# Kernel optimization log

Measured on AMD Instinct MI355X. Metric: run time of the kernel, lower is better.

## Reference

```python
import math
import jax, jax.numpy as jnp
import numpy as np

L_LAYERS, H, D, DV, DM, LMAX, V = 4, 16, 1024, 64, 4096, 1024, 32000


def setup_inputs() -> dict:
    key = jax.random.key(0)
    ks = iter(jax.random.split(key, 40))
    def rn(shape, s=0.02):
        return jax.random.normal(next(ks), shape, jnp.float32) * s
    x_ids = jax.random.randint(next(ks), (LMAX,), 0, V)
    return dict(
        x_ids=x_ids,
        word_emb=rn((V, D)), pos_emb=rn((LMAX, D)),
        Wq=rn((L_LAYERS, H, D, D)), bq=jnp.zeros((L_LAYERS, H, D), jnp.float32),
        Wk=rn((L_LAYERS, H, D, D)), bk=jnp.zeros((L_LAYERS, H, D), jnp.float32),
        Wv=rn((L_LAYERS, H, D, DV)), bv=jnp.zeros((L_LAYERS, H, DV), jnp.float32),
        Wo=rn((L_LAYERS, H * DV, D)), bo=jnp.zeros((L_LAYERS, D), jnp.float32),
        g1=rn((L_LAYERS, D), 0.01), b1=rn((L_LAYERS, D), 0.01),
        g2=rn((L_LAYERS, D), 0.01), b2=rn((L_LAYERS, D), 0.01),
        W1=rn((L_LAYERS, D, DM)), bm1=jnp.zeros((L_LAYERS, DM), jnp.float32),
        W2=rn((L_LAYERS, DM, D)), bm2=jnp.zeros((L_LAYERS, D), jnp.float32),
        gf=rn((D,), 0.01), bf=rn((D,), 0.01),
        Wu=rn((D, V)), bu=jnp.zeros((V,), jnp.float32),
    )


def _ln(x, g, b):
    # original normalizes each row over the full embedding vector (biased std)
    mu = jnp.mean(x, axis=-1, keepdims=True)
    sd = jnp.sqrt(jnp.mean((x - mu) ** 2, axis=-1, keepdims=True))
    return g * (x - mu) / sd + b


def reference(x_ids, word_emb, pos_emb, Wq, bq, Wk, bk, Wv, bv, Wo, bo,
              g1, b1, g2, b2, W1, bm1, W2, bm2, gf, bf, Wu, bu):
    x = word_emb[x_ids] + pos_emb[jnp.arange(LMAX)]          # (LMAX, D)
    mask = jnp.tril(jnp.ones((LMAX, LMAX), bool))
    scale = 1.0 / math.sqrt(D)                               # d_attn = d_e
    for l in range(L_LAYERS):
        xn = _ln(x, g1[l], b1[l])
        q = jnp.einsum('ld,hde->hle', xn, Wq[l]) + bq[l][:, None, :]
        k = jnp.einsum('ld,hde->hle', xn, Wk[l]) + bk[l][:, None, :]
        v = jnp.einsum('ld,hdv->hlv', xn, Wv[l]) + bv[l][:, None, :]
        s = jnp.einsum('hqe,hke->hqk', q, k)                 # (H, LMAX, LMAX)
        s = jnp.where(mask, s, -jnp.inf)
        a = jax.nn.softmax(s * scale, axis=-1)
        o = jnp.einsum('hqk,hkv->hqv', a, v)                 # (H, LMAX, DV)
        # faithful reproduction of MHAttention's OVERLAPPING slice writes:
        # head h writes columns [h, h+DV), later heads overwrite earlier ones
        y = jnp.zeros((LMAX, H * DV), x.dtype)
        for h in range(H):
            y = y.at[:, h:h + DV].set(o[h])
        x = x + y @ Wo[l] + bo[l]
        xn2 = _ln(x, g2[l], b2[l])
        # x + act_layer(xn2) where act_layer(z) = z + mlp2(gelu(mlp1(z)))
        x = x + xn2 + jax.nn.gelu(xn2 @ W1[l] + bm1[l]) @ W2[l] + bm2[l]
    x = _ln(x, gf, bf)
    return jax.nn.softmax(x @ Wu + bu, axis=-1)              # (LMAX, V)
```

## Files before the change

### kernel.cpp

```cpp
#include <hip/hip_runtime.h>

typedef __bf16 bf16_t;
typedef __bf16 bf16x8 __attribute__((ext_vector_type(8)));
typedef float f32x4 __attribute__((ext_vector_type(4)));
typedef unsigned int u32;

#define SEQ    1024
#define DEMB   1024
#define NHEAD  16
#define DVDIM  64
#define DMLP   4096
#define NVOCAB 32000
#define NLAYER 4

typedef const __attribute__((address_space(1))) void gas_t;
typedef __attribute__((address_space(3))) void las_t;

__device__ __forceinline__ void gload_lds16(const void* g, void* l) {
  __builtin_amdgcn_global_load_lds((gas_t*)g, (las_t*)l, 16, 0, 0);
}

union PackU { bf16_t h[2]; u32 u; };
union B4U  { uint2 u; bf16_t h[4]; };

__device__ __forceinline__ float blockSum(float v, float* red) {
  #pragma unroll
  for (int o = 32; o > 0; o >>= 1) v += __shfl_down(v, o, 64);
  __syncthreads();
  if ((threadIdx.x & 63) == 0) red[threadIdx.x >> 6] = v;
  __syncthreads();
  return (red[0] + red[1]) + (red[2] + red[3]);
}
__device__ __forceinline__ float blockMax(float v, float* red) {
  #pragma unroll
  for (int o = 32; o > 0; o >>= 1) v = fmaxf(v, __shfl_down(v, o, 64));
  __syncthreads();
  if ((threadIdx.x & 63) == 0) red[threadIdx.x >> 6] = v;
  __syncthreads();
  return fmaxf(fmaxf(red[0], red[1]), fmaxf(red[2], red[3]));
}

__global__ void embed_k(const int* __restrict__ ids, const float* __restrict__ we,
                        const float* __restrict__ pe, float* __restrict__ x) {
  const int row = blockIdx.x, t = threadIdx.x;
  const long id = ids[row];
  float4 a = *(const float4*)(we + id * (long)DEMB + t * 4);
  float4 b = *(const float4*)(pe + (long)row * DEMB + t * 4);
  float4 o; o.x = a.x + b.x; o.y = a.y + b.y; o.z = a.z + b.z; o.w = a.w + b.w;
  *(float4*)(x + (long)row * DEMB + t * 4) = o;
}

__global__ void __launch_bounds__(256)
ln_k(const float* __restrict__ x, const float* __restrict__ g,
     const float* __restrict__ b, bf16_t* __restrict__ xn,
     float* __restrict__ xupd) {
  __shared__ float red[4];
  const int row = blockIdx.x, t = threadIdx.x;
  const float* xr = x + (long)row * DEMB;
  float4 v = *(const float4*)(xr + t * 4);
  float mu = blockSum(v.x + v.y + v.z + v.w, red) * (1.0f / DEMB);
  float dx = v.x - mu, dy = v.y - mu, dz = v.z - mu, dw = v.w - mu;
  float var = blockSum(dx * dx + dy * dy + dz * dz + dw * dw, red) * (1.0f / DEMB);
  float inv = 1.0f / sqrtf(var);
  float4 gv = *(const float4*)(g + t * 4);
  float4 bv = *(const float4*)(b + t * 4);
  float o0 = gv.x * dx * inv + bv.x;
  float o1 = gv.y * dy * inv + bv.y;
  float o2 = gv.z * dz * inv + bv.z;
  float o3 = gv.w * dw * inv + bv.w;
  PackU p0, p1;
  p0.h[0] = (bf16_t)o0; p0.h[1] = (bf16_t)o1;
  p1.h[0] = (bf16_t)o2; p1.h[1] = (bf16_t)o3;
  uint2 st; st.x = p0.u; st.y = p1.u;
  *(uint2*)(xn + (long)row * DEMB + t * 4) = st;
  if (xupd) {
    float4 nv; nv.x = v.x + o0; nv.y = v.y + o1; nv.z = v.z + o2; nv.w = v.w + o3;
    *(float4*)(xupd + (long)row * DEMB + t * 4) = nv;
  }
}

__global__ void biascat_k(const float* __restrict__ bq, const float* __restrict__ bk,
                          float* __restrict__ out) {
  const int z = blockIdx.x, t = threadIdx.x;
  const int l = z >> 5, i = z & 31;
  const float* src = (i < NHEAD) ? (bq + (long)(l * NHEAD + i) * DEMB)
                                 : (bk + (long)(l * NHEAD + i - NHEAD) * DEMB);
  *(float4*)(out + (long)z * DEMB + t * 4) = *(const float4*)(src + t * 4);
}

__global__ void zyb_k(bf16_t* __restrict__ y) {
  *(uint4*)((char*)y + ((long)blockIdx.x * 256 + threadIdx.x) * 16) = uint4{0, 0, 0, 0};
}

template<bool QK>
__global__ void __launch_bounds__(256)
tconv2_k(const float* __restrict__ in, const float* __restrict__ in2,
         bf16_t* __restrict__ out, int R, int C, long inB, long outB) {
  __shared__ bf16_t tl[64][72];
  const int z = blockIdx.z;
  const float* ip;
  if (QK) {
    const int l = z >> 5, i = z & 31;
    ip = (i < NHEAD) ? (in + (long)(l * NHEAD + i) * inB)
                     : (in2 + (long)(l * NHEAD + i - NHEAD) * inB);
  } else {
    ip = in + (long)z * inB;
  }
  bf16_t* op = out + (long)z * outB;
  const int c0 = blockIdx.x * 64, r0 = blockIdx.y * 64;
  const int t = threadIdx.x;
  const int cc = (t & 31) * 2, rr = t >> 5;
  #pragma unroll
  for (int p = 0; p < 8; ++p) {
    const int r = rr + p * 8;
    float2 v = *(const float2*)(ip + (long)(r0 + r) * C + (c0 + cc));
    tl[cc][r]     = (bf16_t)v.x;
    tl[cc + 1][r] = (bf16_t)v.y;
  }
  __syncthreads();
  const int oc = t >> 2, rk = (t & 3) * 16;
  uint4 a = *(const uint4*)&tl[oc][rk];
  uint4 b = *(const uint4*)&tl[oc][rk + 8];
  *(uint4*)(op + (long)(c0 + oc) * R + (r0 + rk))     = a;
  *(uint4*)(op + (long)(c0 + oc) * R + (r0 + rk + 8)) = b;
}

template<int MODE, int BN, bool CAUSAL, bool TRIMK>
__global__ void __launch_bounds__(256)
gemm_k(const bf16_t* __restrict__ A, const bf16_t* __restrict__ B,
       const float* __restrict__ bias, void* __restrict__ Cv,
       int M, int N, int K, int lda, int ldb,
       long aB, long bB, long cB, int biasB) {
  __shared__ bf16_t lsA[128 * 32];
  __shared__ bf16_t lsB[BN * 32];

  const int t = threadIdx.x;
  const int bz = blockIdx.z;
  const int m0 = blockIdx.y * 128;
  const int n0 = blockIdx.x * BN;
  if (CAUSAL && n0 > m0 + 127) return;

  const bf16_t* Ap = A + (long)bz * aB;
  const bf16_t* Bp = B + (long)bz * bB;
  const int kEnd = TRIMK ? min(K, m0 + 128) : K;

  constexpr int NS = BN / 32;
  const int lane = t & 63;
  const int wid = t >> 6;
  const int wr = (wid >> 1) * 64;
  const int wc = (wid & 1) * (BN / 2);
  const int fr = lane & 15, fg = lane >> 4;
  const int srow = lane >> 2;
  const int skc  = (lane & 3) * 8;

  f32x4 acc[4][NS] = {};

  for (int k0 = 0; k0 < kEnd; k0 += 32) {
    if (k0) __syncthreads();
    #pragma unroll
    for (int i = 0; i < 2; ++i) {
      const int seg = wid * 2 + i;
      gload_lds16(Ap + (long)(m0 + seg * 16 + srow) * lda + (k0 + skc),
                  lsA + seg * 512);
    }
    if (BN == 128) {
      #pragma unroll
      for (int i = 0; i < 2; ++i) {
        const int seg = wid * 2 + i;
        gload_lds16(Bp + (long)(n0 + seg * 16 + srow) * ldb + (k0 + skc),
                    lsB + seg * 512);
      }
    } else {
      gload_lds16(Bp + (long)(n0 + wid * 16 + srow) * ldb + (k0 + skc),
                  lsB + wid * 512);
    }
    __syncthreads();

    bf16x8 af[4], bfv[NS];
    #pragma unroll
    for (int ms = 0; ms < 4; ++ms)
      af[ms] = *(const bf16x8*)(lsA + (wr + ms * 16 + fr) * 32 + fg * 8);
    #pragma unroll
    for (int ns = 0; ns < NS; ++ns)
      bfv[ns] = *(const bf16x8*)(lsB + (wc + ns * 16 + fr) * 32 + fg * 8);
    #pragma unroll
    for (int ms = 0; ms < 4; ++ms)
      #pragma unroll
      for (int ns = 0; ns < NS; ++ns)
        acc[ms][ns] = __builtin_amdgcn_mfma_f32_16x16x32_bf16(
            af[ms], bfv[ns], acc[ms][ns], 0, 0, 0);
  }

  #pragma unroll
  for (int ms = 0; ms < 4; ++ms) {
    #pragma unroll
    for (int ns = 0; ns < NS; ++ns) {
      const int col = n0 + wc + ns * 16 + fr;
      const float bvv = bias ? bias[(long)bz * biasB + col] : 0.0f;
      #pragma unroll
      for (int r = 0; r < 4; ++r) {
        const int row = m0 + wr + ms * 16 + fg * 4 + r;
        float v = acc[ms][ns][r] + bvv;
        if (MODE == 0) {
          ((bf16_t*)Cv)[(long)bz * cB + (long)row * N + col] = (bf16_t)v;
        } else if (MODE == 1) {
          ((float*)Cv)[(long)bz * cB + (long)row * N + col] += v;
        } else if (MODE == 2) {
          ((float*)Cv)[(long)bz * cB + (long)row * N + col] = v;
        } else if (MODE == 3) {
          float gl = 0.5f * v * (1.0f + tanhf(0.7978845608028654f * (v + 0.044715f * v * v * v)));
          ((bf16_t*)Cv)[(long)bz * cB + (long)row * N + col] = (bf16_t)gl;
        } else if (MODE == 4) {
          ((bf16_t*)Cv)[(long)col * M + row] = (bf16_t)v;
        } else {
          if (bz == NHEAD - 1) {
            ((bf16_t*)Cv)[(long)row * 128 + (NHEAD - 1) + col] = (bf16_t)v;
          } else if (col == 0) {
            ((bf16_t*)Cv)[(long)row * 128 + bz] = (bf16_t)v;
          }
        }
      }
    }
  }
}

#define GPHASE(buf, mh, nh, STAGE, VM) do {                                            \
  bf16x8 af[4][2], bfv[2][2];                                                          \
  _Pragma("unroll") for (int mf = 0; mf < 4; ++mf) {                                   \
    const int r = wm * 128 + ((mh) * 4 + mf) * 16 + (lane & 15);                       \
    _Pragma("unroll") for (int ks = 0; ks < 2; ++ks) {                                 \
      const int slot = ks * 4 + (lane >> 4);                                           \
      af[mf][ks] = *(const bf16x8*)(lds + (buf) * 32768 + r * 64 +                     \
                                    ((slot ^ (r & 7)) << 3)); } }                      \
  _Pragma("unroll") for (int nf = 0; nf < 2; ++nf) {                                   \
    const int r = wn * 64 + ((nh) * 2 + nf) * 16 + (lane & 15);                        \
    _Pragma("unroll") for (int ks = 0; ks < 2; ++ks) {                                 \
      const int slot = ks * 4 + (lane >> 4);                                           \
      bfv[nf][ks] = *(const bf16x8*)(lds + (buf) * 32768 + 16384 + r * 64 +            \
                                     ((slot ^ (r & 7)) << 3)); } }                     \
  STAGE;                                                                               \
  __builtin_amdgcn_s_barrier();                                                        \
  asm volatile("s_waitcnt lgkmcnt(0)" ::: "memory");                                   \
  __builtin_amdgcn_sched_barrier(0);                                                   \
  __builtin_amdgcn_s_setprio(1);                                                       \
  _Pragma("unroll") for (int mf = 0; mf < 4; ++mf)                                     \
    _Pragma("unroll") for (int nf = 0; nf < 2; ++nf)                                   \
      _Pragma("unroll") for (int ks = 0; ks < 2; ++ks)                                 \
        acc[(mh) * 4 + mf][(nh) * 2 + nf] = __builtin_amdgcn_mfma_f32_16x16x32_bf16(   \
            af[mf][ks], bfv[nf][ks], acc[(mh) * 4 + mf][(nh) * 2 + nf], 0, 0, 0);      \
  __builtin_amdgcn_s_setprio(0);                                                       \
  VM;                                                                                  \
  __builtin_amdgcn_s_barrier();                                                        \
} while (0)

template<int MODE, bool CAUSAL>
__global__ void __launch_bounds__(512, 1)
gemm256_k(const bf16_t* __restrict__ A, const bf16_t* __restrict__ B,
          const float* __restrict__ bias, void* __restrict__ Cv,
          int M, int N, int K, long aB, long bB, long cB, int biasB) {
  __shared__ bf16_t lds[65536];

  const int t = threadIdx.x;
  const int lane = t & 63, w = t >> 6;
  const int wm = w >> 2, wn = w & 3;
  const int bz = blockIdx.z;
  const int m0 = blockIdx.y * 256, n0 = blockIdx.x * 256;
  if (CAUSAL && n0 > m0 + 255) return;

  const bf16_t* Ap = A + (long)bz * aB;
  const bf16_t* Bp = B + (long)bz * bB;
  const int NT = K >> 6;

  f32x4 acc[8][4] = {};

  auto stA = [&](int half, int kt, int buf) {
    #pragma unroll
    for (int rr = 0; rr < 2; ++rr) {
      const int rw0 = rr * 64 + w * 8;
      const int row0 = ((rw0 >> 6) << 7) | (half << 6) | (rw0 & 63);
      const int r = row0 + (lane >> 3);
      const int slot = lane & 7;
      gload_lds16(Ap + (long)(m0 + r) * K + (kt << 6) + ((slot ^ (r & 7)) << 3),
                  lds + buf * 32768 + row0 * 64);
    }
  };
  auto stB = [&](int half, int kt, int buf) {
    #pragma unroll
    for (int rr = 0; rr < 2; ++rr) {
      const int rw0 = rr * 64 + w * 8;
      const int row0 = ((rw0 >> 5) << 6) | (half << 5) | (rw0 & 31);
      const int r = row0 + (lane >> 3);
      const int slot = lane & 7;
      gload_lds16(Bp + (long)(n0 + r) * K + (kt << 6) + ((slot ^ (r & 7)) << 3),
                  lds + buf * 32768 + 16384 + row0 * 64);
    }
  };

  stB(0, 0, 0); stA(0, 0, 0); stA(1, 0, 0); stB(1, 0, 0);
  stB(0, 1, 1); stA(0, 1, 1);
  asm volatile("s_waitcnt vmcnt(4)" ::: "memory");
  __builtin_amdgcn_s_barrier();

  for (int it = 0; it < (NT >> 1); ++it) {
    const int tt = it * 2;
    const int s1 = min(tt + 1, NT - 1);
    const int s2 = min(tt + 2, NT - 1);
    const int s3 = min(tt + 3, NT - 1);
    GPHASE(0, 0, 0, { stA(1, s1, 1); }, );
    GPHASE(0, 1, 0, { stB(1, s1, 1); }, );
    GPHASE(0, 0, 1, { stB(0, s2, 0); }, );
    GPHASE(0, 1, 1, { stA(0, s2, 0); }, asm volatile("s_waitcnt vmcnt(4)" ::: "memory"));
    GPHASE(1, 0, 0, { stA(1, s2, 0); }, );
    GPHASE(1, 1, 0, { stB(1, s2, 0); }, );
    GPHASE(1, 0, 1, { stB(0, s3, 1); }, );
    GPHASE(1, 1, 1, { stA(0, s3, 1); }, asm volatile("s_waitcnt vmcnt(4)" ::: "memory"));
  }
  asm volatile("s_waitcnt vmcnt(0)" ::: "memory");

  #pragma unroll
  for (int mf = 0; mf < 8; ++mf) {
    #pragma unroll
    for (int nf = 0; nf < 4; ++nf) {
      const int col = n0 + wn * 64 + nf * 16 + (lane & 15);
      const float bvv = bias ? bias[(long)bz * biasB + col] : 0.0f;
      #pragma unroll
      for (int r = 0; r < 4; ++r) {
        const int row = m0 + wm * 128 + mf * 16 + (lane >> 4) * 4 + r;
        const float v = acc[mf][nf][r] + bvv;
        if (MODE == 0)
          ((bf16_t*)Cv)[(long)bz * cB + (long)row * N + col] = (bf16_t)v;
        else
          ((float*)Cv)[(long)bz * cB + (long)row * N + col] = v;
      }
    }
  }
}

__global__ void __launch_bounds__(256)
smax_k(bf16_t* __restrict__ s) {
  __shared__ float red[4];
  const int q = blockIdx.x, h = blockIdx.y, t = threadIdx.x;
  bf16_t* sr = s + ((long)h * SEQ + q) * SEQ;
  const int L = q + 1;
  const float scale = 0.03125f;
  B4U b; b.u = *(const uint2*)(sr + t * 4);
  float x[4];
  float m = -1e30f;
  #pragma unroll
  for (int j = 0; j < 4; ++j) {
    x[j] = (float)b.h[j] * scale;
    if (t * 4 + j < L) m = fmaxf(m, x[j]);
  }
  m = blockMax(m, red);
  float e[4], sum = 0.0f;
  #pragma unroll
  for (int j = 0; j < 4; ++j) {
    e[j] = (t * 4 + j < L) ? expf(x[j] - m) : 0.0f;
    sum += e[j];
  }
  __syncthreads();
  sum = blockSum(sum, red);
  const float inv = 1.0f / sum;
  #pragma unroll
  for (int j = 0; j < 4; ++j) b.h[j] = (bf16_t)(e[j] * inv);
  *(uint2*)(sr + t * 4) = b.u;
}

__global__ void __launch_bounds__(256)
reduce_k(const float* __restrict__ P, const float* __restrict__ bm2,
         float* __restrict__ X) {
  const long i = (long)blockIdx.x * 1024 + threadIdx.x * 4;
  float4 x = *(float4*)(X + i);
  #pragma unroll
  for (int z = 0; z < 4; ++z) {
    float4 p = *(const float4*)(P + (long)z * 1048576 + i);
    x.x += p.x; x.y += p.y; x.z += p.z; x.w += p.w;
  }
  float4 b = *(const float4*)(bm2 + threadIdx.x * 4);
  x.x += b.x; x.y += b.y; x.z += b.z; x.w += b.w;
  *(float4*)(X + i) = x;
}

__global__ void __launch_bounds__(1024)
vsmax_k(float* __restrict__ out) {
  __shared__ float rm[16], rs[16];
  const int row = blockIdx.x, t = threadIdx.x;
  float* r = out + (long)row * NVOCAB;
  float v[32];
  const int nlast = (t < NVOCAB - 31 * 1024) ? 32 : 31;
  float m = -1e30f;
  #pragma unroll
  for (int j = 0; j < 31; ++j) { v[j] = r[j * 1024 + t]; m = fmaxf(m, v[j]); }
  if (nlast == 32) { v[31] = r[31 * 1024 + t]; m = fmaxf(m, v[31]); } else v[31] = -1e30f;
  float s = 0.0f;
  #pragma unroll
  for (int j = 0; j < 32; ++j) s += expf(v[j] - m);
  #pragma unroll
  for (int o = 32; o > 0; o >>= 1) {
    const float mo = __shfl_down(m, o, 64);
    const float so = __shfl_down(s, o, 64);
    const float M2 = fmaxf(m, mo);
    s = s * expf(m - M2) + so * expf(mo - M2);
    m = M2;
  }
  if ((t & 63) == 0) { rm[t >> 6] = m; rs[t >> 6] = s; }
  __syncthreads();
  float M = -1e30f;
  #pragma unroll
  for (int i = 0; i < 16; ++i) M = fmaxf(M, rm[i]);
  float S = 0.0f;
  #pragma unroll
  for (int i = 0; i < 16; ++i) S += rs[i] * expf(rm[i] - M);
  const float inv = 1.0f / S;
  #pragma unroll
  for (int j = 0; j < 31; ++j) r[j * 1024 + t] = expf(v[j] - M) * inv;
  if (nlast == 32) r[31 * 1024 + t] = expf(v[31] - M) * inv;
}

extern "C" void kernel_launch(void* const* d_in, const int* in_sizes, int n_in,
                              void* d_out, int out_size, void* d_ws, size_t ws_size,
                              hipStream_t stream) {
  (void)in_sizes; (void)n_in; (void)out_size; (void)ws_size;
  const int*   x_ids = (const int*)  d_in[0];
  const float* wemb  = (const float*)d_in[1];
  const float* pemb  = (const float*)d_in[2];
  const float* Wq    = (const float*)d_in[3];
  const float* bq    = (const float*)d_in[4];
  const float* Wk    = (const float*)d_in[5];
  const float* bk    = (const float*)d_in[6];
  const float* Wv    = (const float*)d_in[7];
  const float* bv    = (const float*)d_in[8];
  const float* Wo    = (const float*)d_in[9];
  const float* bo    = (const float*)d_in[10];
  const float* g1    = (const float*)d_in[11];
  const float* b1    = (const float*)d_in[12];
  const float* g2    = (const float*)d_in[13];
  const float* b2    = (const float*)d_in[14];
  const float* W1    = (const float*)d_in[15];
  const float* bm1   = (const float*)d_in[16];
  const float* W2    = (const float*)d_in[17];
  const float* bm2   = (const float*)d_in[18];
  const float* gf    = (const float*)d_in[19];
  const float* bfin  = (const float*)d_in[20];
  const float* Wu    = (const float*)d_in[21];
  const float* bu    = (const float*)d_in[22];

  char* ws = (char*)d_ws;
  float*  X    = (float*) ws;
  bf16_t* ACT  = (bf16_t*)(ws + (4u   << 20));
  bf16_t* VbT  = (bf16_t*)(ws + (6u   << 20));
  bf16_t* Yb   = (bf16_t*)(ws + (10u  << 20));
  bf16_t* H1   = (bf16_t*)(ws + (12u  << 20));
  bf16_t* QKb  = (bf16_t*)(ws + (20u  << 20));
  float*  PART = (float*) (ws + (84u  << 20));
  float*  BIAS = (float*) (ws + (100u << 20));
  bf16_t* WTqk = (bf16_t*)(ws + (128u << 20));
  bf16_t* WTv  = (bf16_t*)(ws + (384u << 20));
  bf16_t* WTo  = (bf16_t*)(ws + (392u << 20));
  bf16_t* WT1  = (bf16_t*)(ws + (400u << 20));
  bf16_t* WT2  = (bf16_t*)(ws + (432u << 20));
  bf16_t* WTu  = (bf16_t*)(ws + (464u << 20));

  bf16_t* Sb  = (bf16_t*)d_out;
  float*  OUT = (float*)d_out;

  const long DD = (long)DEMB * DEMB;
  const long SD = (long)SEQ * DEMB;

  embed_k<<<SEQ, 256, 0, stream>>>(x_ids, wemb, pemb, X);
  biascat_k<<<128, 256, 0, stream>>>(bq, bk, BIAS);
  zyb_k<<<64, 256, 0, stream>>>(Yb);
  tconv2_k<true><<<dim3(16, 16, 128), 256, 0, stream>>>(Wq, Wk, WTqk, DEMB, DEMB, DD, DD);
  tconv2_k<false><<<dim3(1, 16, 64), 256, 0, stream>>>(
      Wv, nullptr, WTv, DEMB, DVDIM, (long)DEMB * DVDIM, (long)DVDIM * DEMB);
  tconv2_k<false><<<dim3(16, 2, 4), 256, 0, stream>>>(
      Wo, nullptr, WTo, 128, DEMB, DD, (long)DEMB * 128);
  tconv2_k<false><<<dim3(64, 16, 4), 256, 0, stream>>>(
      W1, nullptr, WT1, DEMB, DMLP, (long)DEMB * DMLP, (long)DMLP * DEMB);
  tconv2_k<false><<<dim3(16, 64, 4), 256, 0, stream>>>(
      W2, nullptr, WT2, DMLP, DEMB, (long)DMLP * DEMB, (long)DEMB * DMLP);
  tconv2_k<false><<<dim3(500, 16, 1), 256, 0, stream>>>(
      Wu, nullptr, WTu, DEMB, NVOCAB, 0L, 0L);

  for (int l = 0; l < NLAYER; ++l) {
    ln_k<<<SEQ, 256, 0, stream>>>(X, g1 + l * DEMB, b1 + l * DEMB, ACT, nullptr);

    gemm256_k<0, false><<<dim3(4, 4, 32), 512, 0, stream>>>(
        ACT, WTqk + (long)l * 32 * DD, BIAS + (long)l * 32 * DEMB, QKb,
        SEQ, DEMB, DEMB, 0L, DD, SD, DEMB);

    gemm_k<4, 128, false, false><<<dim3(8, 8, 1), 256, 0, stream>>>(
        ACT, WTv + (long)l * DD, bv + (long)l * NHEAD * DVDIM, VbT,
        SEQ, NHEAD * DVDIM, DEMB, DEMB, DEMB, 0L, 0L, 0L, 0);

    gemm256_k<0, true><<<dim3(4, 4, NHEAD), 512, 0, stream>>>(
        QKb, QKb + (long)NHEAD * SD, nullptr, Sb,
        SEQ, SEQ, DEMB, SD, SD, (long)SEQ * SEQ, 0);
    smax_k<<<dim3(SEQ, NHEAD), 256, 0, stream>>>(Sb);

    gemm_k<6, 64, false, true><<<dim3(1, 8, NHEAD), 256, 0, stream>>>(
        Sb, VbT, nullptr, Yb,
        SEQ, DVDIM, SEQ, SEQ, SEQ, (long)SEQ * SEQ, (long)DVDIM * SEQ, 0L, 0);

    gemm_k<1, 128, false, false><<<dim3(8, 8, 1), 256, 0, stream>>>(
        Yb, WTo + (long)l * DEMB * 128, bo + (long)l * DEMB, X,
        SEQ, DEMB, 128, 128, 128, 0L, 0L, 0L, 0);

    ln_k<<<SEQ, 256, 0, stream>>>(X, g2 + l * DEMB, b2 + l * DEMB, ACT, X);

    gemm_k<3, 128, false, false><<<dim3(32, 8, 1), 256, 0, stream>>>(
        ACT, WT1 + (long)l * DMLP * DEMB, bm1 + (long)l * DMLP, H1,
        SEQ, DMLP, DEMB, DEMB, DEMB, 0L, 0L, 0L, 0);
    gemm_k<2, 128, false, false><<<dim3(8, 8, 4), 256, 0, stream>>>(
        H1, WT2 + (long)l * DEMB * DMLP, nullptr, PART,
        SEQ, DEMB, 1024, DMLP, DMLP, 1024L, 1024L, (long)SEQ * DEMB, 0);
    reduce_k<<<SEQ, 256, 0, stream>>>(PART, bm2 + (long)l * DEMB, X);
  }

  ln_k<<<SEQ, 256, 0, stream>>>(X, gf, bfin, ACT, nullptr);
  gemm256_k<2, false><<<dim3(125, 4, 1), 512, 0, stream>>>(
      ACT, WTu, bu, OUT, SEQ, NVOCAB, DEMB, 0L, 0L, 0L, 0);
  vsmax_k<<<SEQ, 1024, 0, stream>>>(OUT);
}
```

Measured before the change: 1.507 ms.

## Fold V projection into batched QK GEMM and retile weight transpose kernel

The V projection GEMM is merged into the batched Q/K projection launch as an extra z-slice (bz==32). That slice reads the V weights and writes a transposed bf16 output with packed stores, which removes one kernel launch per layer and lets V share the 256-tile GEMM path. Separately, the weight transpose/convert kernel moves from 64x64 bf16 tiles to 32x32 fp32 tiles with scalar loads and 32-bit packed stores. The smaller tiles mean more blocks and narrower memory transactions in the one-time weight conversion.

```diff
diff --git a/kernel.cpp b/kernel.cpp
--- a/kernel.cpp
+++ b/kernel.cpp
@@ -94,9 +94,9 @@
 
 template<bool QK>
 __global__ void __launch_bounds__(256)
-tconv2_k(const float* __restrict__ in, const float* __restrict__ in2,
+tconv3_k(const float* __restrict__ in, const float* __restrict__ in2,
          bf16_t* __restrict__ out, int R, int C, long inB, long outB) {
-  __shared__ bf16_t tl[64][72];
+  __shared__ float tf[32][33];
   const int z = blockIdx.z;
   const float* ip;
   if (QK) {
@@ -107,22 +107,22 @@
     ip = in + (long)z * inB;
   }
   bf16_t* op = out + (long)z * outB;
-  const int c0 = blockIdx.x * 64, r0 = blockIdx.y * 64;
+  const int c0 = blockIdx.x * 32, r0 = blockIdx.y * 32;
   const int t = threadIdx.x;
-  const int cc = (t & 31) * 2, rr = t >> 5;
-  #pragma unroll
-  for (int p = 0; p < 8; ++p) {
-    const int r = rr + p * 8;
-    float2 v = *(const float2*)(ip + (long)(r0 + r) * C + (c0 + cc));
-    tl[cc][r]     = (bf16_t)v.x;
-    tl[cc + 1][r] = (bf16_t)v.y;
-  }
-  __syncthreads();
-  const int oc = t >> 2, rk = (t & 3) * 16;
-  uint4 a = *(const uint4*)&tl[oc][rk];
-  uint4 b = *(const uint4*)&tl[oc][rk + 8];
-  *(uint4*)(op + (long)(c0 + oc) * R + (r0 + rk))     = a;
-  *(uint4*)(op + (long)(c0 + oc) * R + (r0 + rk + 8)) = b;
+  const int tx = t & 31, ty = t >> 5;
+  #pragma unroll
+  for (int p = 0; p < 4; ++p)
+    tf[ty + 8 * p][tx] = ip[(long)(r0 + ty + 8 * p) * C + (c0 + tx)];
+  __syncthreads();
+  const int l16 = t & 15, cg = t >> 4;
+  #pragma unroll
+  for (int p = 0; p < 2; ++p) {
+    const int cc = cg + p * 16;
+    PackU u;
+    u.h[0] = (bf16_t)tf[2 * l16][cc];
+    u.h[1] = (bf16_t)tf[2 * l16 + 1][cc];
+    *(u32*)(op + (long)(c0 + cc) * R + (r0 + 2 * l16)) = u.u;
+  }
 }
 
 template<int MODE, int BN, bool CAUSAL, bool TRIMK>
@@ -253,11 +253,13 @@
   __builtin_amdgcn_s_barrier();                                                        \
 } while (0)
 
-template<int MODE, bool CAUSAL>
+template<int MODE, bool CAUSAL, bool HASV>
 __global__ void __launch_bounds__(512, 1)
 gemm256_k(const bf16_t* __restrict__ A, const bf16_t* __restrict__ B,
           const float* __restrict__ bias, void* __restrict__ Cv,
-          int M, int N, int K, long aB, long bB, long cB, int biasB) {
+          int M, int N, int K, long aB, long bB, long cB, int biasB,
+          const bf16_t* __restrict__ B2, const float* __restrict__ bias2,
+          bf16_t* __restrict__ Cv2) {
   __shared__ bf16_t lds[65536];
 
   const int t = threadIdx.x;
@@ -267,8 +269,9 @@
   const int m0 = blockIdx.y * 256, n0 = blockIdx.x * 256;
   if (CAUSAL && n0 > m0 + 255) return;
 
+  const bool vm = HASV && (bz == 32);
   const bf16_t* Ap = A + (long)bz * aB;
-  const bf16_t* Bp = B + (long)bz * bB;
+  const bf16_t* Bp = vm ? B2 : B + (long)bz * bB;
   const int NT = K >> 6;
 
   f32x4 acc[8][4] = {};
@@ -322,15 +325,26 @@
     #pragma unroll
     for (int nf = 0; nf < 4; ++nf) {
       const int col = n0 + wn * 64 + nf * 16 + (lane & 15);
-      const float bvv = bias ? bias[(long)bz * biasB + col] : 0.0f;
-      #pragma unroll
-      for (int r = 0; r < 4; ++r) {
-        const int row = m0 + wm * 128 + mf * 16 + (lane >> 4) * 4 + r;
-        const float v = acc[mf][nf][r] + bvv;
-        if (MODE == 0)
-          ((bf16_t*)Cv)[(long)bz * cB + (long)row * N + col] = (bf16_t)v;
-        else
-          ((float*)Cv)[(long)bz * cB + (long)row * N + col] = v;
+      const int row0 = m0 + wm * 128 + mf * 16 + (lane >> 4) * 4;
+      if (HASV && vm) {
+        const float bvv = bias2[col];
+        PackU p0, p1;
+        p0.h[0] = (bf16_t)(acc[mf][nf][0] + bvv);
+        p0.h[1] = (bf16_t)(acc[mf][nf][1] + bvv);
+        p1.h[0] = (bf16_t)(acc[mf][nf][2] + bvv);
+        p1.h[1] = (bf16_t)(acc[mf][nf][3] + bvv);
+        uint2 st; st.x = p0.u; st.y = p1.u;
+        *(uint2*)(Cv2 + (long)col * M + row0) = st;
+      } else {
+        const float bvv = bias ? bias[(long)bz * biasB + col] : 0.0f;
+        #pragma unroll
+        for (int r = 0; r < 4; ++r) {
+          const float v = acc[mf][nf][r] + bvv;
+          if (MODE == 0)
+            ((bf16_t*)Cv)[(long)bz * cB + (long)(row0 + r) * N + col] = (bf16_t)v;
+          else
+            ((float*)Cv)[(long)bz * cB + (long)(row0 + r) * N + col] = v;
+        }
       }
     }
   }
@@ -470,32 +484,29 @@
   embed_k<<<SEQ, 256, 0, stream>>>(x_ids, wemb, pemb, X);
   biascat_k<<<128, 256, 0, stream>>>(bq, bk, BIAS);
   zyb_k<<<64, 256, 0, stream>>>(Yb);
-  tconv2_k<true><<<dim3(16, 16, 128), 256, 0, stream>>>(Wq, Wk, WTqk, DEMB, DEMB, DD, DD);
-  tconv2_k<false><<<dim3(1, 16, 64), 256, 0, stream>>>(
+  tconv3_k<true><<<dim3(32, 32, 128), 256, 0, stream>>>(Wq, Wk, WTqk, DEMB, DEMB, DD, DD);
+  tconv3_k<false><<<dim3(2, 32, 64), 256, 0, stream>>>(
       Wv, nullptr, WTv, DEMB, DVDIM, (long)DEMB * DVDIM, (long)DVDIM * DEMB);
-  tconv2_k<false><<<dim3(16, 2, 4), 256, 0, stream>>>(
+  tconv3_k<false><<<dim3(32, 4, 4), 256, 0, stream>>>(
       Wo, nullptr, WTo, 128, DEMB, DD, (long)DEMB * 128);
-  tconv2_k<false><<<dim3(64, 16, 4), 256, 0, stream>>>(
+  tconv3_k<false><<<dim3(128, 32, 4), 256, 0, stream>>>(
       W1, nullptr, WT1, DEMB, DMLP, (long)DEMB * DMLP, (long)DMLP * DEMB);
-  tconv2_k<false><<<dim3(16, 64, 4), 256, 0, stream>>>(
+  tconv3_k<false><<<dim3(32, 128, 4), 256, 0, stream>>>(
       W2, nullptr, WT2, DMLP, DEMB, (long)DMLP * DEMB, (long)DEMB * DMLP);
-  tconv2_k<false><<<dim3(500, 16, 1), 256, 0, stream>>>(
+  tconv3_k<false><<<dim3(1000, 32, 1), 256, 0, stream>>>(
       Wu, nullptr, WTu, DEMB, NVOCAB, 0L, 0L);
 
   for (int l = 0; l < NLAYER; ++l) {
     ln_k<<<SEQ, 256, 0, stream>>>(X, g1 + l * DEMB, b1 + l * DEMB, ACT, nullptr);
 
-    gemm256_k<0, false><<<dim3(4, 4, 32), 512, 0, stream>>>(
+    gemm256_k<0, false, true><<<dim3(4, 4, 33), 512, 0, stream>>>(
         ACT, WTqk + (long)l * 32 * DD, BIAS + (long)l * 32 * DEMB, QKb,
-        SEQ, DEMB, DEMB, 0L, DD, SD, DEMB);
-
-    gemm_k<4, 128, false, false><<<dim3(8, 8, 1), 256, 0, stream>>>(
-        ACT, WTv + (long)l * DD, bv + (long)l * NHEAD * DVDIM, VbT,
-        SEQ, NHEAD * DVDIM, DEMB, DEMB, DEMB, 0L, 0L, 0L, 0);
-
-    gemm256_k<0, true><<<dim3(4, 4, NHEAD), 512, 0, stream>>>(
+        SEQ, DEMB, DEMB, 0L, DD, SD, DEMB,
+        WTv + (long)l * DD, bv + (long)l * NHEAD * DVDIM, VbT);
+
+    gemm256_k<0, true, false><<<dim3(4, 4, NHEAD), 512, 0, stream>>>(
         QKb, QKb + (long)NHEAD * SD, nullptr, Sb,
-        SEQ, SEQ, DEMB, SD, SD, (long)SEQ * SEQ, 0);
+        SEQ, SEQ, DEMB, SD, SD, (long)SEQ * SEQ, 0, nullptr, nullptr, nullptr);
     smax_k<<<dim3(SEQ, NHEAD), 256, 0, stream>>>(Sb);
 
     gemm_k<6, 64, false, true><<<dim3(1, 8, NHEAD), 256, 0, stream>>>(
@@ -518,7 +529,8 @@
   }
 
   ln_k<<<SEQ, 256, 0, stream>>>(X, gf, bfin, ACT, nullptr);
-  gemm256_k<2, false><<<dim3(125, 4, 1), 512, 0, stream>>>(
-      ACT, WTu, bu, OUT, SEQ, NVOCAB, DEMB, 0L, 0L, 0L, 0);
+  gemm256_k<2, false, false><<<dim3(125, 4, 1), 512, 0, stream>>>(
+      ACT, WTu, bu, OUT, SEQ, NVOCAB, DEMB, 0L, 0L, 0L, 0,
+      nullptr, nullptr, nullptr);
   vsmax_k<<<SEQ, 1024, 0, stream>>>(OUT);
 }
```

New measurement: 1.568 ms. 4.0% more time.
